# Performance work log

Measured on AMD Instinct MI355X. Metric: run time of the kernel, lower is better.

Reference implementation:

```python
import jax, jax.numpy as jnp
import numpy as np

B, C, N = 2, 1024, 80
D = 3 * C + 2  # 3074 token dim
DFF = 2048     # torch TransformerEncoderLayer default dim_feedforward
HW = 224
REFINE = 3
EPS = 1e-5


def _layernorm(x, g, b):
    m = jnp.mean(x, axis=-1, keepdims=True)
    v = jnp.mean((x - m) ** 2, axis=-1, keepdims=True)
    return g * (x - m) / jnp.sqrt(v + EPS) + b


def _pos_encoding(seq_len, dim):
    pos = jnp.arange(seq_len, dtype=jnp.float32)[:, None]
    div = jnp.exp(jnp.arange(0, dim, 2, dtype=jnp.float32) * (-np.log(10000.0) / dim))
    pe = jnp.zeros((seq_len, dim), dtype=jnp.float32)
    pe = pe.at[:, 0::2].set(jnp.sin(pos * div)).at[:, 1::2].set(jnp.cos(pos * div))
    return pe


def _forward(pre_f, curr_f, first_f, ln_g, ln_b, ipw, ipb, opw, opb,
             n1g, n1b, l1w, l1b, l2w, l2b, n2g, n2b, ow, ob,
             prev_b, first_b):
    # --- vectorized find_best_shift: batched circular L1 correlation ---
    idx = (jnp.arange(N)[None, :] - jnp.arange(N)[:, None]) % N  # [shift, pos]
    rolled = first_b[:, idx]                                     # [B, N, N, 2]
    dist = jnp.abs(prev_b[:, None] - rolled).sum(axis=(-1, -2))  # [B, N]
    best = jnp.argmin(dist, axis=1)                              # first min, like torch loop
    roll_idx = (jnp.arange(N)[None, :] - best[:, None]) % N      # [B, N]
    first_b = jax.vmap(lambda fb, ri: fb[ri])(first_b, roll_idx)

    # --- bilinear upsample to 224x224 (F.interpolate, align_corners=False) ---
    up = lambda f: jax.image.resize(f, (f.shape[0], f.shape[1], HW, HW), method='bilinear')
    pre_up, curr_up, first_up = up(pre_f), up(curr_f), up(first_f)

    # --- vectorized get_bou_features: [B,N,C] gather ---
    gather = jax.vmap(lambda f, b: f[:, b[:, 0], b[:, 1]].T)
    pre_q = gather(pre_up, prev_b)      # [B, N, C]
    first_q = gather(first_up, first_b)  # [B, N, C]

    pe = _pos_encoding(N, D)
    curr = prev_b.astype(jnp.float32)
    scale = 1.0 / jnp.sqrt(jnp.float32(D))
    results = []
    for _ in range(REFINE):
        bf = gather(curr_up, curr.astype(jnp.int32))          # [B, N, C]
        tokens = jnp.concatenate([pre_q, bf, curr, first_q], axis=-1)  # [B, N, D]
        tokens = _layernorm(tokens, ln_g, ln_b)
        tokens = tokens + pe[None]
        # --- TransformerEncoderLayer (post-norm, nhead=1, relu, eval/no dropout) ---
        qkv = tokens @ ipw.T + ipb
        q, k, v = jnp.split(qkv, 3, axis=-1)
        attn = jax.nn.softmax(jnp.einsum('bqd,bkd->bqk', q, k) * scale, axis=-1)
        a = jnp.einsum('bqk,bkd->bqd', attn, v) @ opw.T + opb
        x = _layernorm(tokens + a, n1g, n1b)
        ff = jax.nn.relu(x @ l1w.T + l1b) @ l2w.T + l2b
        x = _layernorm(x + ff, n2g, n2b)
        out = x @ ow.T + ob                                   # [B, N, 1026]
        curr = jnp.clip(curr + out[..., C:], 0.0, 223.0)
        pre_q = pre_q + out[..., :C]
        results.append(curr)
    return jnp.stack(results)  # [REFINE, B, N, 2]


def setup_inputs() -> dict:
    key = jax.random.key(0)
    ks = jax.random.split(key, 12)
    f = lambda i, s: jax.random.normal(ks[i], s, dtype=jnp.float32)
    w = lambda i, s: 0.02 * jax.random.normal(ks[i], s, dtype=jnp.float32)
    return {
        'pre_img_features': f(0, (B, C, 14, 14)),
        'curr_img_features': f(1, (B, C, 14, 14)),
        'first_img_features': f(2, (B, C, 14, 14)),
        'previous_boundary': jax.random.randint(ks[3], (B, N, 2), 0, HW),
        'first_boundary': jax.random.randint(ks[4], (B, N, 2), 0, HW),
        'ln_g': jnp.ones((D,), jnp.float32), 'ln_b': jnp.zeros((D,), jnp.float32),
        'in_proj_w': w(5, (3 * D, D)), 'in_proj_b': jnp.zeros((3 * D,), jnp.float32),
        'out_proj_w': w(6, (D, D)), 'out_proj_b': jnp.zeros((D,), jnp.float32),
        'norm1_g': jnp.ones((D,), jnp.float32), 'norm1_b': jnp.zeros((D,), jnp.float32),
        'lin1_w': w(7, (DFF, D)), 'lin1_b': jnp.zeros((DFF,), jnp.float32),
        'lin2_w': w(8, (D, DFF)), 'lin2_b': jnp.zeros((D,), jnp.float32),
        'norm2_g': jnp.ones((D,), jnp.float32), 'norm2_b': jnp.zeros((D,), jnp.float32),
        'out_w': w(9, (C + 2, D)), 'out_b': jnp.zeros((C + 2,), jnp.float32),
    }


def reference(pre_img_features, curr_img_features, first_img_features,
              previous_boundary, first_boundary,
              ln_g, ln_b, in_proj_w, in_proj_b, out_proj_w, out_proj_b,
              norm1_g, norm1_b, lin1_w, lin1_b, lin2_w, lin2_b,
              norm2_g, norm2_b, out_w, out_b):
    return _forward(pre_img_features, curr_img_features, first_img_features,
                    ln_g, ln_b, in_proj_w, in_proj_b, out_proj_w, out_proj_b,
                    norm1_g, norm1_b, lin1_w, lin1_b, lin2_w, lin2_b,
                    norm2_g, norm2_b, out_w, out_b,
                    previous_boundary, first_boundary)
```

## Files before the change

kernel.cpp:

```cpp
#include <hip/hip_runtime.h>
#include <math.h>

#define B_    2
#define C_    1024
#define N_    80
#define D_    3074
#define DFF_  2048
#define OD_   1026
#define QKV_  9222
#define M_    160
#define EPS_  1e-5f
#define KPD_  3104

typedef __attribute__((ext_vector_type(8))) short bf16x8;
typedef __attribute__((ext_vector_type(4))) float f32x4;

__device__ inline short f2bf(float f) {
    unsigned u = __float_as_uint(f);
    u += 0x7fffu + ((u >> 16) & 1u);
    return (short)(u >> 16);
}

__device__ inline float wave_sum(float v) {
#pragma unroll
    for (int off = 32; off > 0; off >>= 1) v += __shfl_down(v, off, 64);
    return v;
}

__device__ inline float wave_max(float v) {
#pragma unroll
    for (int off = 32; off > 0; off >>= 1) v = fmaxf(v, __shfl_down(v, off, 64));
    return v;
}

__device__ inline void block_reduce_2(float& s, float& s2, float* red) {
    int tid = threadIdx.x;
    int lane = tid & 63, wid = tid >> 6;
    s = wave_sum(s);
    s2 = wave_sum(s2);
    if (lane == 0) { red[wid] = s; red[4 + wid] = s2; }
    __syncthreads();
    if (tid == 0) {
        red[8] = red[0] + red[1] + red[2] + red[3];
        red[9] = red[4] + red[5] + red[6] + red[7];
    }
    __syncthreads();
    s = red[8]; s2 = red[9];
}

__device__ inline void bilin_setup(int p, int& i0, int& i1, float& t) {
    float s = (p + 0.5f) * 0.0625f - 0.5f;
    s = fminf(fmaxf(s, 0.0f), 13.0f);
    i0 = (int)s;
    t = s - (float)i0;
    i1 = min(i0 + 1, 13);
}

__device__ inline float bilin_tap(const float* f, int y0, int y1, float ty,
                                  int x0, int x1, float tx) {
    float a = f[y0 * 14 + x0], b = f[y0 * 14 + x1];
    float c = f[y1 * 14 + x0], d = f[y1 * 14 + x1];
    return (1.f - ty) * ((1.f - tx) * a + tx * b) + ty * ((1.f - tx) * c + tx * d);
}

__global__ __launch_bounds__(128) void align_kernel(const int* __restrict__ prev_b,
                                                    const int* __restrict__ first_b,
                                                    int* __restrict__ fb_al) {
    int b = blockIdx.x;
    int tid = threadIdx.x;
    __shared__ int dist[N_];
    __shared__ int bestIdx;
    if (tid < N_) {
        int s = 0;
        for (int j = 0; j < N_; ++j) {
            int src = (j - tid) % N_;
            if (src < 0) src += N_;
            int dy = prev_b[(b * N_ + j) * 2] - first_b[(b * N_ + src) * 2];
            int dx = prev_b[(b * N_ + j) * 2 + 1] - first_b[(b * N_ + src) * 2 + 1];
            s += abs(dy) + abs(dx);
        }
        dist[tid] = s;
    }
    __syncthreads();
    if (tid == 0) {
        int best = 0, bd = dist[0];
        for (int i = 1; i < N_; ++i)
            if (dist[i] < bd) { bd = dist[i]; best = i; }
        bestIdx = best;
    }
    __syncthreads();
    if (tid < N_) {
        int src = (tid - bestIdx) % N_;
        if (src < 0) src += N_;
        fb_al[(b * N_ + tid) * 2]     = first_b[(b * N_ + src) * 2];
        fb_al[(b * N_ + tid) * 2 + 1] = first_b[(b * N_ + src) * 2 + 1];
    }
}

__global__ __launch_bounds__(256) void gather_init_kernel(
        const float* __restrict__ pre_f, const float* __restrict__ first_f,
        const int* __restrict__ prev_b, const int* __restrict__ fb_al,
        float* __restrict__ pre_q, float* __restrict__ first_q,
        float* __restrict__ curr) {
    int m = blockIdx.x;
    int b = m / N_;
    int tid = threadIdx.x;
    int py = prev_b[m * 2], px = prev_b[m * 2 + 1];
    int fy = fb_al[m * 2], fx = fb_al[m * 2 + 1];
    int py0, py1, px0, px1, fy0, fy1, fx0, fx1;
    float pty, ptx, fty, ftx;
    bilin_setup(py, py0, py1, pty);
    bilin_setup(px, px0, px1, ptx);
    bilin_setup(fy, fy0, fy1, fty);
    bilin_setup(fx, fx0, fx1, ftx);
    for (int c = tid; c < C_; c += 256) {
        const float* fp = pre_f + (size_t)(b * C_ + c) * 196;
        const float* ff = first_f + (size_t)(b * C_ + c) * 196;
        pre_q[(size_t)m * C_ + c]   = bilin_tap(fp, py0, py1, pty, px0, px1, ptx);
        first_q[(size_t)m * C_ + c] = bilin_tap(ff, fy0, fy1, fty, fx0, fx1, ftx);
    }
    if (tid < 2) curr[m * 2 + tid] = (float)prev_b[m * 2 + tid];
}

__global__ __launch_bounds__(256) void tokens_kernel(
        const float* __restrict__ curr_f, const float* __restrict__ pre_q,
        const float* __restrict__ first_q, const float* __restrict__ curr,
        const float* __restrict__ ln_g, const float* __restrict__ ln_b,
        float* __restrict__ tokens, short* __restrict__ tokens_bf) {
    int m = blockIdx.x;
    int b = m / N_;
    int n = m % N_;
    int tid = threadIdx.x;
    __shared__ float bf[C_];
    __shared__ float red[10];

    float cy = curr[m * 2], cx = curr[m * 2 + 1];
    int iy = (int)cy, ix = (int)cx;
    int y0, y1, x0, x1;
    float ty, tx;
    bilin_setup(iy, y0, y1, ty);
    bilin_setup(ix, x0, x1, tx);
    for (int c = tid; c < C_; c += 256) {
        const float* f = curr_f + (size_t)(b * C_ + c) * 196;
        bf[c] = bilin_tap(f, y0, y1, ty, x0, x1, tx);
    }
    __syncthreads();

    float s = 0.f, s2 = 0.f;
    for (int d = tid; d < D_; d += 256) {
        float v;
        if (d < C_)            v = pre_q[(size_t)m * C_ + d];
        else if (d < 2 * C_)   v = bf[d - C_];
        else if (d == 2 * C_)  v = cy;
        else if (d == 2*C_+1)  v = cx;
        else                   v = first_q[(size_t)m * C_ + (d - 2 * C_ - 2)];
        s += v; s2 += v * v;
    }
    block_reduce_2(s, s2, red);
    float mean = s / (float)D_;
    float var = s2 / (float)D_ - mean * mean;
    float inv = rsqrtf(var + EPS_);

    const float negLogDivD = -logf(10000.0f) / (float)D_;
    for (int d = tid; d < KPD_; d += 256) {
        if (d < D_) {
            float v;
            if (d < C_)            v = pre_q[(size_t)m * C_ + d];
            else if (d < 2 * C_)   v = bf[d - C_];
            else if (d == 2 * C_)  v = cy;
            else if (d == 2*C_+1)  v = cx;
            else                   v = first_q[(size_t)m * C_ + (d - 2 * C_ - 2)];
            float ln = ln_g[d] * (v - mean) * inv + ln_b[d];
            int kk = d >> 1;
            float ang = (float)n * expf((float)(2 * kk) * negLogDivD);
            float pe = (d & 1) ? cosf(ang) : sinf(ang);
            float val = ln + pe;
            tokens[(size_t)m * D_ + d] = val;
            tokens_bf[(size_t)m * KPD_ + d] = f2bf(val);
        } else {
            tokens_bf[(size_t)m * KPD_ + d] = 0;
        }
    }
}

__global__ __launch_bounds__(256) void gemm_mfma_sk(
        const short* __restrict__ A, const float* __restrict__ Wf,
        const float* __restrict__ bias, float* __restrict__ Cout,
        int K, int KpA, int O, int KC) {
    int kc0 = blockIdx.y * KC;
    if (kc0 >= K) return;
    int kend = min(K, kc0 + KC);

    int lane = threadIdx.x & 63;
    int wave = threadIdx.x >> 6;
    int col  = lane & 15;
    int quad = lane >> 4;
    int o0 = blockIdx.x * 128 + wave * 32 + col;
    int o1 = o0 + 16;
    int oc0 = min(o0, O - 1), oc1 = min(o1, O - 1);

    const float* wrow0 = Wf + (size_t)oc0 * K + quad * 8;
    const float* wrow1 = Wf + (size_t)oc1 * K + quad * 8;
    const short* abase = A + (size_t)col * KpA + quad * 8;

    f32x4 acc0[10], acc1[10];
#pragma unroll
    for (int t = 0; t < 10; ++t)
#pragma unroll
        for (int r = 0; r < 4; ++r) { acc0[t][r] = 0.f; acc1[t][r] = 0.f; }

    int nfull = (kend - kc0) >> 5;
    bf16x8 aCur[10];
    float2 wCur[8];
    if (nfull > 0) {
#pragma unroll
        for (int t = 0; t < 10; ++t)
            aCur[t] = *(const bf16x8*)(abase + (size_t)t * 16 * KpA + kc0);
#pragma unroll
        for (int j = 0; j < 4; ++j) {
            wCur[j]     = *(const float2*)(wrow0 + kc0 + 2 * j);
            wCur[4 + j] = *(const float2*)(wrow1 + kc0 + 2 * j);
        }
    }
    for (int i = 0; i < nfull; ++i) {
        bf16x8 aNxt[10];
        float2 wNxt[8];
        if (i + 1 < nfull) {
            int kn = kc0 + (i + 1) * 32;
#pragma unroll
            for (int t = 0; t < 10; ++t)
                aNxt[t] = *(const bf16x8*)(abase + (size_t)t * 16 * KpA + kn);
#pragma unroll
            for (int j = 0; j < 4; ++j) {
                wNxt[j]     = *(const float2*)(wrow0 + kn + 2 * j);
                wNxt[4 + j] = *(const float2*)(wrow1 + kn + 2 * j);
            }
        }
        bf16x8 b0, b1;
#pragma unroll
        for (int j = 0; j < 4; ++j) {
            b0[2*j] = f2bf(wCur[j].x);     b0[2*j+1] = f2bf(wCur[j].y);
            b1[2*j] = f2bf(wCur[4+j].x);   b1[2*j+1] = f2bf(wCur[4+j].y);
        }
#pragma unroll
        for (int t = 0; t < 10; ++t) {
            acc0[t] = __builtin_amdgcn_mfma_f32_16x16x32_bf16(aCur[t], b0, acc0[t], 0, 0, 0);
            acc1[t] = __builtin_amdgcn_mfma_f32_16x16x32_bf16(aCur[t], b1, acc1[t], 0, 0, 0);
        }
#pragma unroll
        for (int t = 0; t < 10; ++t) aCur[t] = aNxt[t];
#pragma unroll
        for (int j = 0; j < 8; ++j) wCur[j] = wNxt[j];
    }
    int kmain = kc0 + nfull * 32;
    if (kmain < kend) {
        bf16x8 b0, b1;
#pragma unroll
        for (int j = 0; j < 8; ++j) {
            int k = kmain + quad * 8 + j;
            b0[j] = (k < kend) ? f2bf(Wf[(size_t)oc0 * K + k]) : (short)0;
            b1[j] = (k < kend) ? f2bf(Wf[(size_t)oc1 * K + k]) : (short)0;
        }
#pragma unroll
        for (int t = 0; t < 10; ++t) {
            bf16x8 af = *(const bf16x8*)(abase + (size_t)t * 16 * KpA + kmain);
            acc0[t] = __builtin_amdgcn_mfma_f32_16x16x32_bf16(af, b0, acc0[t], 0, 0, 0);
            acc1[t] = __builtin_amdgcn_mfma_f32_16x16x32_bf16(af, b1, acc1[t], 0, 0, 0);
        }
    }
    if (o0 < O) {
        float bv = (blockIdx.y == 0) ? bias[o0] : 0.f;
#pragma unroll
        for (int t = 0; t < 10; ++t)
#pragma unroll
            for (int r = 0; r < 4; ++r)
                atomicAdd(&Cout[(size_t)(t * 16 + quad * 4 + r) * O + o0], acc0[t][r] + bv);
    }
    if (o1 < O) {
        float bv = (blockIdx.y == 0) ? bias[o1] : 0.f;
#pragma unroll
        for (int t = 0; t < 10; ++t)
#pragma unroll
            for (int r = 0; r < 4; ++r)
                atomicAdd(&Cout[(size_t)(t * 16 + quad * 4 + r) * O + o1], acc1[t][r] + bv);
    }
}

__global__ __launch_bounds__(256) void relu_cvt_kernel(const float* __restrict__ in,
                                                       short* __restrict__ out,
                                                       int n) {
    int i = blockIdx.x * 256 + threadIdx.x;
    if (i < n) out[i] = f2bf(fmaxf(in[i], 0.f));
}

__global__ __launch_bounds__(256) void qkv_cvt_kernel(const float* __restrict__ qkv,
                                                      short* __restrict__ q_bf,
                                                      short* __restrict__ k_bf,
                                                      short* __restrict__ v_bf) {
    int m = blockIdx.x;
    int b = m / N_, q = m % N_;
    const float* src = qkv + (size_t)m * QKV_;
    for (int d = threadIdx.x; d < KPD_; d += 256) {
        short qv = (d < D_) ? f2bf(src[d])          : (short)0;
        short kv = (d < D_) ? f2bf(src[D_ + d])     : (short)0;
        short vv = (d < D_) ? f2bf(src[2 * D_ + d]) : (short)0;
        q_bf[(size_t)m * KPD_ + d] = qv;
        k_bf[(size_t)m * KPD_ + d] = kv;
        v_bf[((size_t)b * 96 + q) * KPD_ + d] = vv;
    }
}

__global__ __launch_bounds__(256) void scores_mfma(const short* __restrict__ q_bf,
                                                   const short* __restrict__ k_bf,
                                                   float* __restrict__ sc) {
    int bi = blockIdx.x;
    int b = bi / 25, qt = (bi % 25) / 5, kt = bi % 5;
    int lane = threadIdx.x & 63, wave = threadIdx.x >> 6;
    int col = lane & 15, quad = lane >> 4;
    const short* qbase = q_bf + (size_t)(b * N_ + qt * 16 + col) * KPD_ + quad * 8;
    const short* kbase = k_bf + (size_t)(b * N_ + kt * 16 + col) * KPD_ + quad * 8;
    f32x4 acc;
#pragma unroll
    for (int r = 0; r < 4; ++r) acc[r] = 0.f;
    int c0 = wave * 25, c1 = min(97, c0 + 25);
    for (int c = c0; c < c1; ++c) {
        bf16x8 af = *(const bf16x8*)(qbase + c * 32);
        bf16x8 bf8 = *(const bf16x8*)(kbase + c * 32);
        acc = __builtin_amdgcn_mfma_f32_16x16x32_bf16(af, bf8, acc, 0, 0, 0);
    }
    __shared__ f32x4 red[4][64];
    red[wave][lane] = acc;
    __syncthreads();
    if (threadIdx.x < 64) {
        f32x4 t = red[0][lane];
#pragma unroll
        for (int w = 1; w < 4; ++w)
#pragma unroll
            for (int r = 0; r < 4; ++r) t[r] += red[w][lane][r];
        float scale = rsqrtf((float)D_);
#pragma unroll
        for (int r = 0; r < 4; ++r)
            sc[(size_t)(b * N_ + qt * 16 + quad * 4 + r) * N_ + kt * 16 + col] = t[r] * scale;
    }
}

__global__ __launch_bounds__(256) void softmax_kernel(const float* __restrict__ sc,
                                                      short* __restrict__ p_bf) {
    int m = blockIdx.x * 4 + (threadIdx.x >> 6);
    int lane = threadIdx.x & 63;
    const float* row = sc + (size_t)m * N_;
    float a = row[lane];
    float bv = (lane < 16) ? row[64 + lane] : -1e30f;
    float mx = wave_max(fmaxf(a, bv));
    mx = __shfl(mx, 0, 64);
    float e0 = expf(a - mx);
    float e1 = (lane < 16) ? expf(bv - mx) : 0.f;
    float sum = wave_sum(e0 + e1);
    sum = __shfl(sum, 0, 64);
    float rs = 1.0f / sum;
    p_bf[(size_t)m * 96 + lane] = f2bf(e0 * rs);
    if (lane < 32)
        p_bf[(size_t)m * 96 + 64 + lane] = (lane < 16) ? f2bf(e1 * rs) : (short)0;
}

__global__ __launch_bounds__(256) void av_mfma(const short* __restrict__ p_bf,
                                               const short* __restrict__ v_bf,
                                               short* __restrict__ av_bf) {
    int bi = blockIdx.x;
    int b = bi / 49, g = bi % 49;
    int lane = threadIdx.x & 63, wave = threadIdx.x >> 6;
    int dtile = g * 4 + wave;
    if (dtile >= 194) return;
    int d0 = dtile * 16;
    int col = lane & 15, quad = lane >> 4;
    const short* pbase = p_bf + (size_t)b * N_ * 96 + quad * 8;
    const short* vb = v_bf + (size_t)b * 96 * KPD_ + d0 + col;
    f32x4 acc[5];
#pragma unroll
    for (int t = 0; t < 5; ++t)
#pragma unroll
        for (int r = 0; r < 4; ++r) acc[t][r] = 0.f;
#pragma unroll
    for (int c = 0; c < 3; ++c) {
        bf16x8 bf8;
#pragma unroll
        for (int j = 0; j < 8; ++j)
            bf8[j] = vb[(size_t)(c * 32 + quad * 8 + j) * KPD_];
#pragma unroll
        for (int t = 0; t < 5; ++t) {
            bf16x8 af = *(const bf16x8*)(pbase + (size_t)(t * 16 + col) * 96 + c * 32);
            acc[t] = __builtin_amdgcn_mfma_f32_16x16x32_bf16(af, bf8, acc[t], 0, 0, 0);
        }
    }
#pragma unroll
    for (int t = 0; t < 5; ++t)
#pragma unroll
        for (int r = 0; r < 4; ++r)
            av_bf[(size_t)(b * N_ + t * 16 + quad * 4 + r) * KPD_ + d0 + col] = f2bf(acc[t][r]);
}

template <bool WF32>
__global__ __launch_bounds__(256) void ln_kernel(const float* __restrict__ xin,
                                                 const float* __restrict__ res,
                                                 const float* __restrict__ g,
                                                 const float* __restrict__ bta,
                                                 float* __restrict__ outf,
                                                 short* __restrict__ outb) {
    int m = blockIdx.x;
    int tid = threadIdx.x;
    __shared__ float red[10];
    const float* xr = xin + (size_t)m * D_;
    const float* rr = res + (size_t)m * D_;
    float s = 0.f, s2 = 0.f;
    for (int d = tid; d < D_; d += 256) {
        float v = xr[d] + rr[d];
        s += v; s2 += v * v;
    }
    block_reduce_2(s, s2, red);
    float mean = s / (float)D_;
    float var = s2 / (float)D_ - mean * mean;
    float inv = rsqrtf(var + EPS_);
    for (int d = tid; d < KPD_; d += 256) {
        if (d < D_) {
            float v = xr[d] + rr[d];
            float y = g[d] * (v - mean) * inv + bta[d];
            if (WF32) outf[(size_t)m * D_ + d] = y;
            outb[(size_t)m * KPD_ + d] = f2bf(y);
        } else {
            outb[(size_t)m * KPD_ + d] = 0;
        }
    }
}

__global__ __launch_bounds__(256) void update_kernel(const float* __restrict__ outb,
                                                     float* __restrict__ curr,
                                                     float* __restrict__ pre_q,
                                                     float* __restrict__ results) {
    int m = blockIdx.x;
    int tid = threadIdx.x;
    for (int c = tid; c < C_; c += 256)
        pre_q[(size_t)m * C_ + c] += outb[(size_t)m * OD_ + c];
    if (tid < 2) {
        float nc = curr[m * 2 + tid] + outb[(size_t)m * OD_ + C_ + tid];
        nc = fminf(fmaxf(nc, 0.f), 223.f);
        curr[m * 2 + tid] = nc;
        results[m * 2 + tid] = nc;
    }
}

extern "C" void kernel_launch(void* const* d_in, const int* in_sizes, int n_in,
                              void* d_out, int out_size, void* d_ws, size_t ws_size,
                              hipStream_t stream) {
    const float* pre_f   = (const float*)d_in[0];
    const float* curr_f  = (const float*)d_in[1];
    const float* first_f = (const float*)d_in[2];
    const int*   prev_b  = (const int*)d_in[3];
    const int*   first_b = (const int*)d_in[4];
    const float* ln_g    = (const float*)d_in[5];
    const float* ln_b    = (const float*)d_in[6];
    const float* ipw     = (const float*)d_in[7];
    const float* ipb     = (const float*)d_in[8];
    const float* opw     = (const float*)d_in[9];
    const float* opb     = (const float*)d_in[10];
    const float* n1g     = (const float*)d_in[11];
    const float* n1b     = (const float*)d_in[12];
    const float* l1w     = (const float*)d_in[13];
    const float* l1b     = (const float*)d_in[14];
    const float* l2w     = (const float*)d_in[15];
    const float* l2b     = (const float*)d_in[16];
    const float* n2g     = (const float*)d_in[17];
    const float* n2b     = (const float*)d_in[18];
    const float* ow      = (const float*)d_in[19];
    const float* ob      = (const float*)d_in[20];
    float* outp = (float*)d_out;

    float* wf = (float*)d_ws;
    size_t off = 0;
    int*   fb_al   = (int*)(wf + off); off += 320;
    float* curr    = wf + off;         off += 320;
    float* pre_q   = wf + off;         off += (size_t)M_ * C_;
    float* first_q = wf + off;         off += (size_t)M_ * C_;
    float* tokens  = wf + off;         off += (size_t)M_ * D_;
    float* qkv     = wf + off;         off += (size_t)M_ * QKV_;
    float* aout    = wf + off;         off += (size_t)M_ * D_;
    float* xbuf    = wf + off;         off += (size_t)M_ * D_;
    float* ff1f    = wf + off;         off += (size_t)M_ * DFF_;
    float* ffout   = wf + off;         off += (size_t)M_ * D_;
    float* outb    = wf + off;         off += (size_t)M_ * OD_;
    float* sc      = wf + off;         off += (size_t)M_ * N_;
    short* tokens_bf = (short*)(wf + off); off += (size_t)M_ * KPD_ / 2;
    short* x_bf      = (short*)(wf + off); off += (size_t)M_ * KPD_ / 2;
    short* x2_bf     = (short*)(wf + off); off += (size_t)M_ * KPD_ / 2;
    short* av_bf     = (short*)(wf + off); off += (size_t)M_ * KPD_ / 2;
    short* ff1_bf    = (short*)(wf + off); off += (size_t)M_ * DFF_ / 2;
    short* q_bf      = (short*)(wf + off); off += (size_t)M_ * KPD_ / 2;
    short* k_bf      = (short*)(wf + off); off += (size_t)M_ * KPD_ / 2;
    short* v_bf      = (short*)(wf + off); off += (size_t)B_ * 96 * KPD_ / 2;
    short* p_bf      = (short*)(wf + off); off += (size_t)M_ * 96 / 2;
    (void)ws_size; (void)in_sizes; (void)n_in; (void)out_size;

    hipLaunchKernelGGL(align_kernel, dim3(B_), dim3(128), 0, stream,
                       prev_b, first_b, fb_al);
    hipLaunchKernelGGL(gather_init_kernel, dim3(M_), dim3(256), 0, stream,
                       pre_f, first_f, prev_b, fb_al, pre_q, first_q, curr);
    hipMemsetAsync(v_bf, 0, (size_t)B_ * 96 * KPD_ * 2, stream);

    for (int it = 0; it < 3; ++it) {
        hipMemsetAsync(qkv,   0, (size_t)M_ * QKV_ * 4, stream);
        hipMemsetAsync(aout,  0, (size_t)M_ * D_   * 4, stream);
        hipMemsetAsync(ff1f,  0, (size_t)M_ * DFF_ * 4, stream);
        hipMemsetAsync(ffout, 0, (size_t)M_ * D_   * 4, stream);
        hipMemsetAsync(outb,  0, (size_t)M_ * OD_  * 4, stream);

        hipLaunchKernelGGL(tokens_kernel, dim3(M_), dim3(256), 0, stream,
                           curr_f, pre_q, first_q, curr, ln_g, ln_b, tokens, tokens_bf);
        hipLaunchKernelGGL(gemm_mfma_sk, dim3(73, 6), dim3(256), 0, stream,
                           tokens_bf, ipw, ipb, qkv, D_, KPD_, QKV_, 544);
        hipLaunchKernelGGL(qkv_cvt_kernel, dim3(M_), dim3(256), 0, stream,
                           qkv, q_bf, k_bf, v_bf);
        hipLaunchKernelGGL(scores_mfma, dim3(50), dim3(256), 0, stream,
                           q_bf, k_bf, sc);
        hipLaunchKernelGGL(softmax_kernel, dim3(40), dim3(256), 0, stream,
                           sc, p_bf);
        hipLaunchKernelGGL(av_mfma, dim3(98), dim3(256), 0, stream,
                           p_bf, v_bf, av_bf);
        hipLaunchKernelGGL(gemm_mfma_sk, dim3(25, 10), dim3(256), 0, stream,
                           av_bf, opw, opb, aout, D_, KPD_, D_, 320);
        hipLaunchKernelGGL((ln_kernel<true>), dim3(M_), dim3(256), 0, stream,
                           tokens, aout, n1g, n1b, xbuf, x_bf);
        hipLaunchKernelGGL(gemm_mfma_sk, dim3(16, 17), dim3(256), 0, stream,
                           x_bf, l1w, l1b, ff1f, D_, KPD_, DFF_, 192);
        hipLaunchKernelGGL(relu_cvt_kernel, dim3((M_ * DFF_ + 255) / 256), dim3(256), 0, stream,
                           ff1f, ff1_bf, M_ * DFF_);
        hipLaunchKernelGGL(gemm_mfma_sk, dim3(25, 11), dim3(256), 0, stream,
                           ff1_bf, l2w, l2b, ffout, DFF_, DFF_, D_, 192);
        hipLaunchKernelGGL((ln_kernel<false>), dim3(M_), dim3(256), 0, stream,
                           xbuf, ffout, n2g, n2b, (float*)nullptr, x2_bf);
        hipLaunchKernelGGL(gemm_mfma_sk, dim3(9, 13), dim3(256), 0, stream,
                           x2_bf, ow, ob, outb, D_, KPD_, OD_, 256);
        hipLaunchKernelGGL(update_kernel, dim3(M_), dim3(256), 0, stream,
                           outb, curr, pre_q, outp + (size_t)it * M_ * 2);
    }
}
```

Before: 1.189 ms.

## Pre-convert GEMM weights to padded bf16 once and use bf16 split-K GEMM

Adds a one-time kernel that converts each fp32 weight matrix to a K-padded bf16 copy in workspace, then runs a new GEMM that loads bf16 weights directly with register double-buffering. The intent is to halve weight traffic across the three refinement iterations and drop per-load conversion, with more split-K chunks for parallelism. The conversion is paid on every call, costs extra workspace, and adds more atomic adds. The new path runs only if the workspace is large enough, otherwise the old fp32-weight path is used.

```diff
diff --git a/kernel.cpp b/kernel.cpp
--- a/kernel.cpp
+++ b/kernel.cpp
@@ -180,6 +180,94 @@
         } else {
             tokens_bf[(size_t)m * KPD_ + d] = 0;
         }
+    }
+}
+
+__global__ __launch_bounds__(256) void wcvt_kernel(const float* __restrict__ w,
+                                                   short* __restrict__ o,
+                                                   int K, int Kp) {
+    int r = blockIdx.x;
+    const float* src = w + (size_t)r * K;
+    short* dst = o + (size_t)r * Kp;
+    int nv = K >> 2;
+    int npv = Kp >> 2;
+    for (int g = threadIdx.x; g < npv; g += 256) {
+        short4 ov;
+        if (g < nv) {
+            float2 a = *(const float2*)(src + 4 * g);
+            float2 b = *(const float2*)(src + 4 * g + 2);
+            ov.x = f2bf(a.x); ov.y = f2bf(a.y);
+            ov.z = f2bf(b.x); ov.w = f2bf(b.y);
+        } else {
+            float v0 = (4 * g     < K) ? src[4 * g]     : 0.f;
+            float v1 = (4 * g + 1 < K) ? src[4 * g + 1] : 0.f;
+            float v2 = (4 * g + 2 < K) ? src[4 * g + 2] : 0.f;
+            float v3 = (4 * g + 3 < K) ? src[4 * g + 3] : 0.f;
+            ov.x = f2bf(v0); ov.y = f2bf(v1); ov.z = f2bf(v2); ov.w = f2bf(v3);
+        }
+        *(short4*)(dst + 4 * g) = ov;
+    }
+}
+
+__global__ __launch_bounds__(256, 3) void gemm_mfma_bf(
+        const short* __restrict__ A, const short* __restrict__ Wb,
+        const float* __restrict__ bias, float* __restrict__ Cout,
+        int Kp, int O, int KC) {
+    int kc0 = blockIdx.y * KC;
+    if (kc0 >= Kp) return;
+    int kend = min(Kp, kc0 + KC);
+
+    int lane = threadIdx.x & 63;
+    int wave = threadIdx.x >> 6;
+    int col  = lane & 15;
+    int quad = lane >> 4;
+    int o0 = blockIdx.x * 128 + wave * 32 + col;
+    int o1 = o0 + 16;
+    int oc0 = min(o0, O - 1), oc1 = min(o1, O - 1);
+
+    const short* w0p = Wb + (size_t)oc0 * Kp + quad * 8 + kc0;
+    const short* w1p = Wb + (size_t)oc1 * Kp + quad * 8 + kc0;
+    const short* ap  = A  + (size_t)col * Kp + quad * 8 + kc0;
+
+    f32x4 acc0[10], acc1[10];
+#pragma unroll
+    for (int t = 0; t < 10; ++t)
+#pragma unroll
+        for (int r = 0; r < 4; ++r) { acc0[t][r] = 0.f; acc1[t][r] = 0.f; }
+
+    int nch = (kend - kc0) >> 5;
+    bf16x8 w0c = *(const bf16x8*)(w0p);
+    bf16x8 w1c = *(const bf16x8*)(w1p);
+    for (int i = 0; i < nch; ++i) {
+        bf16x8 w0n, w1n;
+        if (i + 1 < nch) {
+            w0n = *(const bf16x8*)(w0p + (i + 1) * 32);
+            w1n = *(const bf16x8*)(w1p + (i + 1) * 32);
+        }
+#pragma unroll
+        for (int t = 0; t < 10; ++t) {
+            bf16x8 af = *(const bf16x8*)(ap + (size_t)t * 16 * Kp + i * 32);
+            acc0[t] = __builtin_amdgcn_mfma_f32_16x16x32_bf16(af, w0c, acc0[t], 0, 0, 0);
+            acc1[t] = __builtin_amdgcn_mfma_f32_16x16x32_bf16(af, w1c, acc1[t], 0, 0, 0);
+        }
+        w0c = w0n; w1c = w1n;
+    }
+
+    if (o0 < O) {
+        float bv = (blockIdx.y == 0) ? bias[o0] : 0.f;
+#pragma unroll
+        for (int t = 0; t < 10; ++t)
+#pragma unroll
+            for (int r = 0; r < 4; ++r)
+                atomicAdd(&Cout[(size_t)(t * 16 + quad * 4 + r) * O + o0], acc0[t][r] + bv);
+    }
+    if (o1 < O) {
+        float bv = (blockIdx.y == 0) ? bias[o1] : 0.f;
+#pragma unroll
+        for (int t = 0; t < 10; ++t)
+#pragma unroll
+            for (int r = 0; r < 4; ++r)
+                atomicAdd(&Cout[(size_t)(t * 16 + quad * 4 + r) * O + o1], acc1[t][r] + bv);
     }
 }
 
@@ -497,13 +585,27 @@
     short* k_bf      = (short*)(wf + off); off += (size_t)M_ * KPD_ / 2;
     short* v_bf      = (short*)(wf + off); off += (size_t)B_ * 96 * KPD_ / 2;
     short* p_bf      = (short*)(wf + off); off += (size_t)M_ * 96 / 2;
-    (void)ws_size; (void)in_sizes; (void)n_in; (void)out_size;
+    short* ipw_bf = (short*)(wf + off); off += (size_t)QKV_ * KPD_ / 2;
+    short* opw_bf = (short*)(wf + off); off += (size_t)D_ * KPD_ / 2;
+    short* l1w_bf = (short*)(wf + off); off += (size_t)DFF_ * KPD_ / 2;
+    short* l2w_bf = (short*)(wf + off); off += (size_t)D_ * DFF_ / 2;
+    short* ow_bf  = (short*)(wf + off); off += (size_t)OD_ * KPD_ / 2;
+    bool use_bf = ws_size >= off * sizeof(float);
+    (void)in_sizes; (void)n_in; (void)out_size;
 
     hipLaunchKernelGGL(align_kernel, dim3(B_), dim3(128), 0, stream,
                        prev_b, first_b, fb_al);
     hipLaunchKernelGGL(gather_init_kernel, dim3(M_), dim3(256), 0, stream,
                        pre_f, first_f, prev_b, fb_al, pre_q, first_q, curr);
     hipMemsetAsync(v_bf, 0, (size_t)B_ * 96 * KPD_ * 2, stream);
+
+    if (use_bf) {
+        hipLaunchKernelGGL(wcvt_kernel, dim3(QKV_), dim3(256), 0, stream, ipw, ipw_bf, D_, KPD_);
+        hipLaunchKernelGGL(wcvt_kernel, dim3(D_),   dim3(256), 0, stream, opw, opw_bf, D_, KPD_);
+        hipLaunchKernelGGL(wcvt_kernel, dim3(DFF_), dim3(256), 0, stream, l1w, l1w_bf, D_, KPD_);
+        hipLaunchKernelGGL(wcvt_kernel, dim3(D_),   dim3(256), 0, stream, l2w, l2w_bf, DFF_, DFF_);
+        hipLaunchKernelGGL(wcvt_kernel, dim3(OD_),  dim3(256), 0, stream, ow, ow_bf, D_, KPD_);
+    }
 
     for (int it = 0; it < 3; ++it) {
         hipMemsetAsync(qkv,   0, (size_t)M_ * QKV_ * 4, stream);
@@ -514,8 +616,12 @@
 
         hipLaunchKernelGGL(tokens_kernel, dim3(M_), dim3(256), 0, stream,
                            curr_f, pre_q, first_q, curr, ln_g, ln_b, tokens, tokens_bf);
-        hipLaunchKernelGGL(gemm_mfma_sk, dim3(73, 6), dim3(256), 0, stream,
-                           tokens_bf, ipw, ipb, qkv, D_, KPD_, QKV_, 544);
+        if (use_bf)
+            hipLaunchKernelGGL(gemm_mfma_bf, dim3(73, 11), dim3(256), 0, stream,
+                               tokens_bf, ipw_bf, ipb, qkv, KPD_, QKV_, 288);
+        else
+            hipLaunchKernelGGL(gemm_mfma_sk, dim3(73, 6), dim3(256), 0, stream,
+                               tokens_bf, ipw, ipb, qkv, D_, KPD_, QKV_, 544);
         hipLaunchKernelGGL(qkv_cvt_kernel, dim3(M_), dim3(256), 0, stream,
                            qkv, q_bf, k_bf, v_bf);
         hipLaunchKernelGGL(scores_mfma, dim3(50), dim3(256), 0, stream,
@@ -524,20 +630,36 @@
                            sc, p_bf);
         hipLaunchKernelGGL(av_mfma, dim3(98), dim3(256), 0, stream,
                            p_bf, v_bf, av_bf);
-        hipLaunchKernelGGL(gemm_mfma_sk, dim3(25, 10), dim3(256), 0, stream,
-                           av_bf, opw, opb, aout, D_, KPD_, D_, 320);
+        if (use_bf)
+            hipLaunchKernelGGL(gemm_mfma_bf, dim3(25, 20), dim3(256), 0, stream,
+                               av_bf, opw_bf, opb, aout, KPD_, D_, 160);
+        else
+            hipLaunchKernelGGL(gemm_mfma_sk, dim3(25, 10), dim3(256), 0, stream,
+                               av_bf, opw, opb, aout, D_, KPD_, D_, 320);
         hipLaunchKernelGGL((ln_kernel<true>), dim3(M_), dim3(256), 0, stream,
                            tokens, aout, n1g, n1b, xbuf, x_bf);
-        hipLaunchKernelGGL(gemm_mfma_sk, dim3(16, 17), dim3(256), 0, stream,
-                           x_bf, l1w, l1b, ff1f, D_, KPD_, DFF_, 192);
+        if (use_bf)
+            hipLaunchKernelGGL(gemm_mfma_bf, dim3(16, 25), dim3(256), 0, stream,
+                               x_bf, l1w_bf, l1b, ff1f, KPD_, DFF_, 128);
+        else
+            hipLaunchKernelGGL(gemm_mfma_sk, dim3(16, 17), dim3(256), 0, stream,
+                               x_bf, l1w, l1b, ff1f, D_, KPD_, DFF_, 192);
         hipLaunchKernelGGL(relu_cvt_kernel, dim3((M_ * DFF_ + 255) / 256), dim3(256), 0, stream,
                            ff1f, ff1_bf, M_ * DFF_);
-        hipLaunchKernelGGL(gemm_mfma_sk, dim3(25, 11), dim3(256), 0, stream,
-                           ff1_bf, l2w, l2b, ffout, DFF_, DFF_, D_, 192);
+        if (use_bf)
+            hipLaunchKernelGGL(gemm_mfma_bf, dim3(25, 16), dim3(256), 0, stream,
+                               ff1_bf, l2w_bf, l2b, ffout, DFF_, D_, 128);
+        else
+            hipLaunchKernelGGL(gemm_mfma_sk, dim3(25, 11), dim3(256), 0, stream,
+                               ff1_bf, l2w, l2b, ffout, DFF_, DFF_, D_, 192);
         hipLaunchKernelGGL((ln_kernel<false>), dim3(M_), dim3(256), 0, stream,
                            xbuf, ffout, n2g, n2b, (float*)nullptr, x2_bf);
-        hipLaunchKernelGGL(gemm_mfma_sk, dim3(9, 13), dim3(256), 0, stream,
-                           x2_bf, ow, ob, outb, D_, KPD_, OD_, 256);
+        if (use_bf)
+            hipLaunchKernelGGL(gemm_mfma_bf, dim3(9, 25), dim3(256), 0, stream,
+                               x2_bf, ow_bf, ob, outb, KPD_, OD_, 128);
+        else
+            hipLaunchKernelGGL(gemm_mfma_sk, dim3(9, 13), dim3(256), 0, stream,
+                               x2_bf, ow, ob, outb, D_, KPD_, OD_, 256);
         hipLaunchKernelGGL(update_kernel, dim3(M_), dim3(256), 0, stream,
                            outb, curr, pre_q, outp + (size_t)it * M_ * 2);
     }
```

Result: slower. 1.517 ms (+27.6%).

## Pre-pack weights to bf16 MFMA layout and add packed-weight GEMM

Applied to the files above, without the earlier changes.

Adds a one-time packing pass per call that converts each fp32 weight matrix into bf16 tiles in MFMA fragment order, then runs a new GEMM that reads these packed tiles with one wave per k-range and a shared-memory reduction. The aim is to cut weight bandwidth in half and avoid converting weights on every refinement iteration, and the new grid splits work over output strips and M groups. It costs extra workspace and a per-call packing pass over every weight matrix. The path runs only if the workspace is large enough, otherwise the old GEMM is kept.

```diff
diff --git a/kernel.cpp b/kernel.cpp
--- a/kernel.cpp
+++ b/kernel.cpp
@@ -179,6 +179,105 @@
             tokens_bf[(size_t)m * KPD_ + d] = f2bf(val);
         } else {
             tokens_bf[(size_t)m * KPD_ + d] = 0;
+        }
+    }
+}
+
+__global__ __launch_bounds__(256) void wpack_kernel(const float* __restrict__ w,
+                                                    short* __restrict__ o,
+                                                    int K, int O, int nch) {
+    int s = blockIdx.x;
+    int items = nch * 64;
+    for (int idx = threadIdx.x; idx < items; idx += 256) {
+        int c = idx >> 6, l = idx & 63;
+        int col = l & 15, quad = l >> 4;
+        int orow = s * 16 + col;
+        int k0 = c * 32 + quad * 8;
+        bf16x8 v;
+        if (orow < O && k0 + 8 <= K) {
+            const float* src = w + (size_t)orow * K + k0;
+            float2 a = *(const float2*)(src);
+            float2 b = *(const float2*)(src + 2);
+            float2 cc = *(const float2*)(src + 4);
+            float2 d = *(const float2*)(src + 6);
+            v[0] = f2bf(a.x);  v[1] = f2bf(a.y);
+            v[2] = f2bf(b.x);  v[3] = f2bf(b.y);
+            v[4] = f2bf(cc.x); v[5] = f2bf(cc.y);
+            v[6] = f2bf(d.x);  v[7] = f2bf(d.y);
+        } else {
+#pragma unroll
+            for (int j = 0; j < 8; ++j) {
+                int k = k0 + j;
+                v[j] = (orow < O && k < K) ? f2bf(w[(size_t)orow * K + k]) : (short)0;
+            }
+        }
+        *(bf16x8*)(o + ((size_t)s * nch + c) * 512 + l * 8) = v;
+    }
+}
+
+__global__ __launch_bounds__(256) void gemm_pk(
+        const short* __restrict__ A, const short* __restrict__ Wp,
+        const float* __restrict__ bias, float* __restrict__ Cout,
+        int KpA, int nch, int O) {
+    int strip = blockIdx.x;
+    int nsk = gridDim.y;
+    int mg = blockIdx.z;
+    int lane = threadIdx.x & 63, wave = threadIdx.x >> 6;
+    int col = lane & 15, quad = lane >> 4;
+
+    int per = (nch + nsk - 1) / nsk;
+    int cs = blockIdx.y * per;
+    int ce = min(nch, cs + per);
+    if (cs >= ce) return;
+    int tot = ce - cs;
+    int qn = tot >> 2, rmd = tot & 3;
+    int c0 = cs + wave * qn + min(wave, rmd);
+    int c1 = c0 + qn + (wave < rmd ? 1 : 0);
+
+    const short* wp = Wp + (size_t)strip * nch * 512 + lane * 8;
+    const short* ap = A + (size_t)(mg * 80 + col) * KpA + quad * 8;
+
+    f32x4 acc[5];
+#pragma unroll
+    for (int t = 0; t < 5; ++t)
+#pragma unroll
+        for (int r = 0; r < 4; ++r) acc[t][r] = 0.f;
+
+    if (c0 < c1) {
+        bf16x8 wcur = *(const bf16x8*)(wp + (size_t)c0 * 512);
+        for (int c = c0; c < c1; ++c) {
+            bf16x8 wnxt = wcur;
+            if (c + 1 < c1) wnxt = *(const bf16x8*)(wp + (size_t)(c + 1) * 512);
+#pragma unroll
+            for (int t = 0; t < 5; ++t) {
+                bf16x8 af = *(const bf16x8*)(ap + (size_t)t * 16 * KpA + c * 32);
+                acc[t] = __builtin_amdgcn_mfma_f32_16x16x32_bf16(af, wcur, acc[t], 0, 0, 0);
+            }
+            wcur = wnxt;
+        }
+    }
+
+    __shared__ f32x4 red[4][5][64];
+#pragma unroll
+    for (int t = 0; t < 5; ++t) red[wave][t][lane] = acc[t];
+    __syncthreads();
+    for (int item = threadIdx.x; item < 320; item += 256) {
+        int t = item >> 6, l2 = item & 63;
+        f32x4 v = red[0][t][l2];
+#pragma unroll
+        for (int w = 1; w < 4; ++w)
+#pragma unroll
+            for (int r = 0; r < 4; ++r) v[r] += red[w][t][l2][r];
+        int oc = strip * 16 + (l2 & 15);
+        if (oc < O) {
+            float bv = (blockIdx.y == 0) ? bias[oc] : 0.f;
+            int rbase = mg * 80 + t * 16 + (l2 >> 4) * 4;
+#pragma unroll
+            for (int r = 0; r < 4; ++r) {
+                float val = v[r] + bv;
+                if (nsk == 1) Cout[(size_t)(rbase + r) * O + oc] = val;
+                else atomicAdd(&Cout[(size_t)(rbase + r) * O + oc], val);
+            }
         }
     }
 }
@@ -497,7 +596,13 @@
     short* k_bf      = (short*)(wf + off); off += (size_t)M_ * KPD_ / 2;
     short* v_bf      = (short*)(wf + off); off += (size_t)B_ * 96 * KPD_ / 2;
     short* p_bf      = (short*)(wf + off); off += (size_t)M_ * 96 / 2;
-    (void)ws_size; (void)in_sizes; (void)n_in; (void)out_size;
+    short* ipw_pk = (short*)(wf + off); off += (size_t)577 * 97 * 256;
+    short* opw_pk = (short*)(wf + off); off += (size_t)193 * 97 * 256;
+    short* l1w_pk = (short*)(wf + off); off += (size_t)128 * 97 * 256;
+    short* l2w_pk = (short*)(wf + off); off += (size_t)193 * 64 * 256;
+    short* ow_pk  = (short*)(wf + off); off += (size_t)65  * 97 * 256;
+    bool use_bf = ws_size >= off * sizeof(float);
+    (void)in_sizes; (void)n_in; (void)out_size;
 
     hipLaunchKernelGGL(align_kernel, dim3(B_), dim3(128), 0, stream,
                        prev_b, first_b, fb_al);
@@ -505,8 +610,16 @@
                        pre_f, first_f, prev_b, fb_al, pre_q, first_q, curr);
     hipMemsetAsync(v_bf, 0, (size_t)B_ * 96 * KPD_ * 2, stream);
 
+    if (use_bf) {
+        hipLaunchKernelGGL(wpack_kernel, dim3(577), dim3(256), 0, stream, ipw, ipw_pk, D_, QKV_, 97);
+        hipLaunchKernelGGL(wpack_kernel, dim3(193), dim3(256), 0, stream, opw, opw_pk, D_, D_, 97);
+        hipLaunchKernelGGL(wpack_kernel, dim3(128), dim3(256), 0, stream, l1w, l1w_pk, D_, DFF_, 97);
+        hipLaunchKernelGGL(wpack_kernel, dim3(193), dim3(256), 0, stream, l2w, l2w_pk, DFF_, D_, 64);
+        hipLaunchKernelGGL(wpack_kernel, dim3(65),  dim3(256), 0, stream, ow, ow_pk, D_, OD_, 97);
+    }
+
     for (int it = 0; it < 3; ++it) {
-        hipMemsetAsync(qkv,   0, (size_t)M_ * QKV_ * 4, stream);
+        if (!use_bf) hipMemsetAsync(qkv, 0, (size_t)M_ * QKV_ * 4, stream);
         hipMemsetAsync(aout,  0, (size_t)M_ * D_   * 4, stream);
         hipMemsetAsync(ff1f,  0, (size_t)M_ * DFF_ * 4, stream);
         hipMemsetAsync(ffout, 0, (size_t)M_ * D_   * 4, stream);
@@ -514,8 +627,12 @@
 
         hipLaunchKernelGGL(tokens_kernel, dim3(M_), dim3(256), 0, stream,
                            curr_f, pre_q, first_q, curr, ln_g, ln_b, tokens, tokens_bf);
-        hipLaunchKernelGGL(gemm_mfma_sk, dim3(73, 6), dim3(256), 0, stream,
-                           tokens_bf, ipw, ipb, qkv, D_, KPD_, QKV_, 544);
+        if (use_bf)
+            hipLaunchKernelGGL(gemm_pk, dim3(577, 1, 2), dim3(256), 0, stream,
+                               tokens_bf, ipw_pk, ipb, qkv, KPD_, 97, QKV_);
+        else
+            hipLaunchKernelGGL(gemm_mfma_sk, dim3(73, 6), dim3(256), 0, stream,
+                               tokens_bf, ipw, ipb, qkv, D_, KPD_, QKV_, 544);
         hipLaunchKernelGGL(qkv_cvt_kernel, dim3(M_), dim3(256), 0, stream,
                            qkv, q_bf, k_bf, v_bf);
         hipLaunchKernelGGL(scores_mfma, dim3(50), dim3(256), 0, stream,
@@ -524,20 +641,36 @@
                            sc, p_bf);
         hipLaunchKernelGGL(av_mfma, dim3(98), dim3(256), 0, stream,
                            p_bf, v_bf, av_bf);
-        hipLaunchKernelGGL(gemm_mfma_sk, dim3(25, 10), dim3(256), 0, stream,
-                           av_bf, opw, opb, aout, D_, KPD_, D_, 320);
+        if (use_bf)
+            hipLaunchKernelGGL(gemm_pk, dim3(193, 2, 2), dim3(256), 0, stream,
+                               av_bf, opw_pk, opb, aout, KPD_, 97, D_);
+        else
+            hipLaunchKernelGGL(gemm_mfma_sk, dim3(25, 10), dim3(256), 0, stream,
+                               av_bf, opw, opb, aout, D_, KPD_, D_, 320);
         hipLaunchKernelGGL((ln_kernel<true>), dim3(M_), dim3(256), 0, stream,
                            tokens, aout, n1g, n1b, xbuf, x_bf);
-        hipLaunchKernelGGL(gemm_mfma_sk, dim3(16, 17), dim3(256), 0, stream,
-                           x_bf, l1w, l1b, ff1f, D_, KPD_, DFF_, 192);
+        if (use_bf)
+            hipLaunchKernelGGL(gemm_pk, dim3(128, 2, 2), dim3(256), 0, stream,
+                               x_bf, l1w_pk, l1b, ff1f, KPD_, 97, DFF_);
+        else
+            hipLaunchKernelGGL(gemm_mfma_sk, dim3(16, 17), dim3(256), 0, stream,
+                               x_bf, l1w, l1b, ff1f, D_, KPD_, DFF_, 192);
         hipLaunchKernelGGL(relu_cvt_kernel, dim3((M_ * DFF_ + 255) / 256), dim3(256), 0, stream,
                            ff1f, ff1_bf, M_ * DFF_);
-        hipLaunchKernelGGL(gemm_mfma_sk, dim3(25, 11), dim3(256), 0, stream,
-                           ff1_bf, l2w, l2b, ffout, DFF_, DFF_, D_, 192);
+        if (use_bf)
+            hipLaunchKernelGGL(gemm_pk, dim3(193, 2, 2), dim3(256), 0, stream,
+                               ff1_bf, l2w_pk, l2b, ffout, DFF_, 64, D_);
+        else
+            hipLaunchKernelGGL(gemm_mfma_sk, dim3(25, 11), dim3(256), 0, stream,
+                               ff1_bf, l2w, l2b, ffout, DFF_, DFF_, D_, 192);
         hipLaunchKernelGGL((ln_kernel<false>), dim3(M_), dim3(256), 0, stream,
                            xbuf, ffout, n2g, n2b, (float*)nullptr, x2_bf);
-        hipLaunchKernelGGL(gemm_mfma_sk, dim3(9, 13), dim3(256), 0, stream,
-                           x2_bf, ow, ob, outb, D_, KPD_, OD_, 256);
+        if (use_bf)
+            hipLaunchKernelGGL(gemm_pk, dim3(65, 4, 2), dim3(256), 0, stream,
+                               x2_bf, ow_pk, ob, outb, KPD_, 97, OD_);
+        else
+            hipLaunchKernelGGL(gemm_mfma_sk, dim3(9, 13), dim3(256), 0, stream,
+                               x2_bf, ow, ob, outb, D_, KPD_, OD_, 256);
         hipLaunchKernelGGL(update_kernel, dim3(M_), dim3(256), 0, stream,
                            outb, curr, pre_q, outp + (size_t)it * M_ * 2);
     }
```

After: 1.040 ms. -12.5%, faster.
